# Optimization experiments

Hardware: AMD Instinct MI355X
Metric: run time of the kernel (lower is better)

The kernel has to match this reference:

```python
import jax, jax.numpy as jnp
import numpy as np

N = 50000
E_RAND = 800000
IN, HID, OUT = 128, 64, 40
HEADS = (2, 1, 1)
NEG_SLOPE = 0.2


def setup_inputs() -> dict:
    key = jax.random.key(0)
    ks = jax.random.split(key, 16)
    # random edges with src != dst, then append self-loops (remove+add_self_loop)
    src_r = jax.random.randint(ks[0], (E_RAND,), 0, N)
    off = jax.random.randint(ks[1], (E_RAND,), 1, N)
    dst_r = (src_r + off) % N
    loops = jnp.arange(N)
    src = jnp.concatenate([src_r, loops]).astype(jnp.int64)
    dst = jnp.concatenate([dst_r, loops]).astype(jnp.int64)
    in_feat = jax.random.normal(ks[2], (N, IN), dtype=jnp.float32)

    def lin(k, fan_in, fan_out):
        return jax.random.normal(k, (fan_in, fan_out), dtype=jnp.float32) / np.sqrt(fan_in)

    H0, H1, H2 = HEADS
    # layer 0: in=IN, out=HID, heads=H0
    W0 = lin(ks[3], IN, H0 * HID)
    al0 = jax.random.normal(ks[4], (H0, HID), dtype=jnp.float32) * 0.1
    ar0 = jax.random.normal(ks[5], (H0, HID), dtype=jnp.float32) * 0.1
    b0 = jnp.zeros((H0 * HID,), dtype=jnp.float32)
    # layer 1: in=HID*H0, out=HID, heads=H1
    W1 = lin(ks[6], HID * H0, H1 * HID)
    al1 = jax.random.normal(ks[7], (H1, HID), dtype=jnp.float32) * 0.1
    ar1 = jax.random.normal(ks[8], (H1, HID), dtype=jnp.float32) * 0.1
    b1 = jnp.zeros((H1 * HID,), dtype=jnp.float32)
    # layer 2: in=HID*H1, out=OUT, heads=H2
    W2 = lin(ks[9], HID * H1, H2 * OUT)
    al2 = jax.random.normal(ks[10], (H2, OUT), dtype=jnp.float32) * 0.1
    ar2 = jax.random.normal(ks[11], (H2, OUT), dtype=jnp.float32) * 0.1
    b2 = jnp.zeros((H2 * OUT,), dtype=jnp.float32)
    return {"in_feat": in_feat, "src": src, "dst": dst,
            "W0": W0, "al0": al0, "ar0": ar0, "b0": b0,
            "W1": W1, "al1": al1, "ar1": ar1, "b1": b1,
            "W2": W2, "al2": al2, "ar2": ar2, "b2": b2}


def _gat_layer(x, src, dst, W, al, ar, b):
    # x: [N, Fin]; W: [Fin, H*D]; al/ar: [H, D]; b: [H*D]
    H, D = al.shape
    feat = (x @ W).reshape(-1, H, D)                 # [N, H, D]
    el = jnp.sum(feat * al, axis=-1)                 # [N, H]
    er = jnp.sum(feat * ar, axis=-1)                 # [N, H]
    e = jax.nn.leaky_relu(el[src] + er[dst], NEG_SLOPE)  # [E, H]
    m = jax.ops.segment_max(e, dst, num_segments=x.shape[0])
    ee = jnp.exp(e - jax.lax.stop_gradient(m)[dst])
    s = jax.ops.segment_sum(ee, dst, num_segments=x.shape[0])
    alpha = ee / s[dst]                              # softmax over in-edges per dst
    out = jax.ops.segment_sum(feat[src] * alpha[:, :, None], dst,
                              num_segments=x.shape[0])  # [N, H, D]
    return out + b.reshape(1, H, D)


def reference(in_feat, src, dst, W0, al0, ar0, b0, W1, al1, ar1, b1, W2, al2, ar2, b2):
    h = _gat_layer(in_feat, src, dst, W0, al0, ar0, b0).reshape(in_feat.shape[0], -1)  # flatten(1)
    h = _gat_layer(h, src, dst, W1, al1, ar1, b1).mean(axis=1)                          # mean over heads
    h = _gat_layer(h, src, dst, W2, al2, ar2, b2).reshape(in_feat.shape[0], -1)         # flatten(1)
    return h
```

## Files before the change

kernel.cpp:

```cpp
#include <hip/hip_runtime.h>
#include <hip/hip_fp16.h>
#include <math.h>

#define NEG_SLOPE 0.2f

typedef _Float16 h8 __attribute__((ext_vector_type(8)));
typedef float f4 __attribute__((ext_vector_type(4)));


__device__ inline float2 up2(unsigned u) {
    __half2 h;
    __builtin_memcpy(&h, &u, 4);
    return __half22float2(h);
}
__device__ inline unsigned pk2(float a, float b) {
    __half2 h = __floats2half2_rn(a, b);
    unsigned u;
    __builtin_memcpy(&u, &h, 4);
    return u;
}
__device__ inline void fma8(float* acc, const uint4& v, float p) {
    float2 f;
    f = up2(v.x); acc[0] += f.x * p; acc[1] += f.y * p;
    f = up2(v.y); acc[2] += f.x * p; acc[3] += f.y * p;
    f = up2(v.z); acc[4] += f.x * p; acc[5] += f.y * p;
    f = up2(v.w); acc[6] += f.x * p; acc[7] += f.y * p;
}
__device__ inline float dot4(const float4& a, const float4& b) {
    return a.x * b.x + a.y * b.y + a.z * b.z + a.w * b.w;
}


__global__ __launch_bounds__(256) void degree_hist_rank(const int* __restrict__ dst,
                                                        int* __restrict__ deg,
                                                        int* __restrict__ rank, int E) {
    int e = blockIdx.x * blockDim.x + threadIdx.x;
    if (e >= E) return;
    int d = __builtin_nontemporal_load(&dst[e]);
    int r = atomicAdd(&deg[d], 1);
    __builtin_nontemporal_store(r, &rank[e]);
}

__global__ __launch_bounds__(256) void scan_block_sums(const int* __restrict__ in,
                                                       int* __restrict__ partial, int n) {
    int i = blockIdx.x * 256 + threadIdx.x;
    int v = (i < n) ? in[i] : 0;
#pragma unroll
    for (int off = 32; off; off >>= 1) v += __shfl_xor(v, off);
    __shared__ int wsum[4];
    if ((threadIdx.x & 63) == 0) wsum[threadIdx.x >> 6] = v;
    __syncthreads();
    if (threadIdx.x == 0) partial[blockIdx.x] = wsum[0] + wsum[1] + wsum[2] + wsum[3];
}

__global__ __launch_bounds__(256) void scan_offsets(const int* __restrict__ partial,
                                                    int* __restrict__ partial_scan,
                                                    int* __restrict__ total_out, int nb,
                                                    const float* __restrict__ al2,
                                                    const float* __restrict__ ar2,
                                                    float* __restrict__ al2p,
                                                    float* __restrict__ ar2p) {
    __shared__ int buf[256];
    int t = threadIdx.x;
    int v = (t < nb) ? partial[t] : 0;
    buf[t] = v;
    __syncthreads();
    for (int off = 1; off < 256; off <<= 1) {
        int x = (t >= off) ? buf[t - off] : 0;
        __syncthreads();
        buf[t] += x;
        __syncthreads();
    }
    partial_scan[t] = buf[t] - v;
    if (t == 255) *total_out = buf[255];
    if (t < 64) {
        al2p[t] = (t < 40) ? al2[t] : 0.f;
        ar2p[t] = (t < 40) ? ar2[t] : 0.f;
    }
}

__global__ __launch_bounds__(256) void scan_final(const int* __restrict__ in,
                                                  const int* __restrict__ partial_scan,
                                                  int* __restrict__ out, int n) {
    __shared__ int buf[256];
    int t = threadIdx.x;
    int i = blockIdx.x * 256 + t;
    int v = (i < n) ? in[i] : 0;
    buf[t] = v;
    __syncthreads();
    for (int off = 1; off < 256; off <<= 1) {
        int x = (t >= off) ? buf[t - off] : 0;
        __syncthreads();
        buf[t] += x;
        __syncthreads();
    }
    if (i < n) out[i] = partial_scan[blockIdx.x] + buf[t] - v;
}

__global__ __launch_bounds__(256) void scatter_rank(const int* __restrict__ src,
                                                    const int* __restrict__ dst,
                                                    const int* __restrict__ rank,
                                                    const int* __restrict__ row_start,
                                                    int* __restrict__ csr_src, int E) {
    int e = blockIdx.x * blockDim.x + threadIdx.x;
    if (e >= E) return;
    int d = __builtin_nontemporal_load(&dst[e]);
    int s = __builtin_nontemporal_load(&src[e]);
    int r = __builtin_nontemporal_load(&rank[e]);
    csr_src[row_start[d] + r] = s;
}


__global__ __launch_bounds__(256) void pack_w(const float* __restrict__ W0,
                                              const float* __restrict__ W1,
                                              const float* __restrict__ W2,
                                              __half* __restrict__ P0,
                                              __half* __restrict__ P1,
                                              __half* __restrict__ P2) {
    int b = blockIdx.x;
    const float* W;
    __half* P;
    int K, M, Msrc;
    if (b < 8) {
        W = W0; P = P0; K = 128; M = 128; Msrc = 128;
    } else if (b < 12) {
        W = W1; P = P1; K = 128; M = 64; Msrc = 64; b -= 8;
    } else {
        W = W2; P = P2; K = 64; M = 64; Msrc = 40; b -= 12;
    }
    int t = b * 256 + threadIdx.x;
    int nk8 = K >> 3;
    if (t >= M * nk8) return;
    int m = t % M, k8 = t / M;
    int k = k8 * 8;
    int c = m >> 4, s = k >> 5, hi = (k >> 3) & 3, lane = hi * 16 + (m & 15);
    float v[8];
#pragma unroll
    for (int i = 0; i < 8; ++i)
        v[i] = (m < Msrc) ? W[(size_t)(k + i) * Msrc + m] : 0.f;
    uint4 o;
    o.x = pk2(v[0], v[1]);
    o.y = pk2(v[2], v[3]);
    o.z = pk2(v[4], v[5]);
    o.w = pk2(v[6], v[7]);
    *(uint4*)(P + (size_t)((c * (K >> 5) + s) * 64 + lane) * 8) = o;
}


template <int K, int M, int H, bool A16>
__global__ __launch_bounds__(256) void gemm_mfma(const void* __restrict__ xin,
                                                 const __half* __restrict__ Wp,
                                                 const float* __restrict__ al,
                                                 const float* __restrict__ ar,
                                                 __half* __restrict__ outh,
                                                 float* __restrict__ el,
                                                 float* __restrict__ er, int N) {
    constexpr int KS = K / 32;
    constexpr int CF = M / 16;
    constexpr int LDT = 133;
    constexpr int CH8 = M / 8;
    constexpr int NC8 = CH8 / 4;
    __shared__ float tl[4 * 16 * LDT];
    const int tid = threadIdx.x;
    const int wid = tid >> 6, lane = tid & 63;
    const int lhi = lane >> 4, llo = lane & 15;
    const int rowbase = blockIdx.x * 64 + wid * 16;
    float* wt = tl + wid * 16 * LDT;

    f4 acc[CF];
#pragma unroll
    for (int c = 0; c < CF; ++c) acc[c] = f4{0.f, 0.f, 0.f, 0.f};

    const int arow = rowbase + llo;
    const bool aval = arow < N;
#pragma unroll
    for (int s = 0; s < KS; ++s) {
        h8 a = {};
        if (aval) {
            if constexpr (A16) {
                const __half* xp = (const __half*)xin + (size_t)arow * K + s * 32 + lhi * 8;
                a = *(const h8*)xp;
            } else {
                const float4* xp = (const float4*)((const float*)xin + (size_t)arow * K +
                                                   s * 32 + lhi * 8);
                float4 x0 = xp[0];
                float4 x1 = xp[1];
                a[0] = (_Float16)x0.x; a[1] = (_Float16)x0.y;
                a[2] = (_Float16)x0.z; a[3] = (_Float16)x0.w;
                a[4] = (_Float16)x1.x; a[5] = (_Float16)x1.y;
                a[6] = (_Float16)x1.z; a[7] = (_Float16)x1.w;
            }
        }
#pragma unroll
        for (int c = 0; c < CF; ++c) {
            h8 b = *(const h8*)(Wp + (size_t)((c * KS + s) * 64 + lane) * 8);
            acc[c] = __builtin_amdgcn_mfma_f32_16x16x32_f16(a, b, acc[c], 0, 0, 0);
        }
    }

#pragma unroll
    for (int c = 0; c < CF; ++c) {
#pragma unroll
        for (int r = 0; r < 4; ++r)
            wt[(lhi * 4 + r) * LDT + c * 16 + llo] = acc[c][r];
    }

    const int rrow = lane >> 2;
    const int q = lane & 3;
    const int grow = rowbase + rrow;
    float elp[H], erp[H];
#pragma unroll
    for (int h = 0; h < H; ++h) { elp[h] = 0.f; erp[h] = 0.f; }
    const float4* al4 = (const float4*)al;
    const float4* ar4 = (const float4*)ar;
#pragma unroll
    for (int i = 0; i < NC8; ++i) {
        int j8 = q + 4 * i;
        float4 v0 = *(float4*)&wt[rrow * LDT + 8 * j8];
        float4 v1 = *(float4*)&wt[rrow * LDT + 8 * j8 + 4];
        int h = (H == 2 && i >= NC8 / 2) ? 1 : 0;
        float4 a0 = al4[2 * j8], a1 = al4[2 * j8 + 1];
        float4 r0 = ar4[2 * j8], r1 = ar4[2 * j8 + 1];
        elp[h] += dot4(v0, a0) + dot4(v1, a1);
        erp[h] += dot4(v0, r0) + dot4(v1, r1);
        if (grow < N) {
            uint4 pkv;
            pkv.x = pk2(v0.x, v0.y);
            pkv.y = pk2(v0.z, v0.w);
            pkv.z = pk2(v1.x, v1.y);
            pkv.w = pk2(v1.z, v1.w);
            *(uint4*)(outh + (size_t)grow * M + 8 * j8) = pkv;
        }
    }
#pragma unroll
    for (int h = 0; h < H; ++h) {
#pragma unroll
        for (int off = 1; off < 4; off <<= 1) {
            elp[h] += __shfl_xor(elp[h], off);
            erp[h] += __shfl_xor(erp[h], off);
        }
    }
    if (q == 0 && grow < N) {
        if constexpr (H == 2) {
            *(float2*)&el[(size_t)grow * 2] = float2{elp[0], elp[1]};
            *(float2*)&er[(size_t)grow * 2] = float2{erp[0], erp[1]};
        } else {
            el[grow] = elp[0];
            er[grow] = erp[0];
        }
    }
}


template <int H, int D, int FSTRIDE, int T, bool OUT16>
__global__ __launch_bounds__(256) void gat_aggregate(const __half* __restrict__ feat,
                                                     const float* __restrict__ el,
                                                     const float* __restrict__ er,
                                                     const int* __restrict__ row_start,
                                                     const int* __restrict__ csr_src,
                                                     const float* __restrict__ bias,
                                                     void* __restrict__ out, int N) {
    constexpr int NLp = FSTRIDE / 8;
    constexpr int Gn = 64 / NLp;
    constexpr int BATCH = Gn * T;
    constexpr int WL = (H * D) / 8;
    static_assert(BATCH <= 64 && 64 % NLp == 0, "layout");
    int dstn = (blockIdx.x * blockDim.x + threadIdx.x) >> 6;
    int lane = threadIdx.x & 63;
    if (dstn >= N) return;
    int beg = row_start[dstn], end = row_start[dstn + 1];
    int cnt = end - beg;

    float er_d[H];
#pragma unroll
    for (int h = 0; h < H; ++h) er_d[h] = er[(size_t)dstn * H + h];

    float ssum[H];
    float acc8[8];
#pragma unroll
    for (int h = 0; h < H; ++h) ssum[h] = 0.f;
#pragma unroll
    for (int i = 0; i < 8; ++i) acc8[i] = 0.f;

    const int g = lane / NLp;
    const int ln = lane % NLp;

    auto gather = [&](int s_reg, const float p_reg[H], int j, int limit) {
        uint4 v[T];
#pragma unroll
        for (int t = 0; t < T; ++t) {
            if (j + Gn * t < limit) {
                int sj = __shfl(s_reg, j + Gn * t + g);
                v[t] = ((const uint4*)(feat + (size_t)sj * FSTRIDE))[ln];
            }
        }
#pragma unroll
        for (int t = 0; t < T; ++t) {
            if (j + Gn * t < limit) {
                int slot = j + Gn * t + g;
                float pj = __shfl(p_reg[0], slot);
                if constexpr (H == 2) {
                    float pj1 = __shfl(p_reg[1], slot);
                    pj = (ln >= 8) ? pj1 : pj;
                }
                fma8(acc8, v[t], pj);
            }
        }
    };

    if (cnt <= 64) {
        int idx = beg + lane;
        bool valid = idx < end;
        int s = valid ? csr_src[idx] : csr_src[beg];
        float ev[H], p[H];
        if constexpr (H == 2) {
            float2 e2 = ((const float2*)el)[s];
            ev[0] = e2.x + er_d[0];
            ev[1] = e2.y + er_d[1];
        } else {
            ev[0] = el[s] + er_d[0];
        }
#pragma unroll
        for (int h = 0; h < H; ++h) {
            float e = ev[h];
            e = (e > 0.f) ? e : NEG_SLOPE * e;
            p[h] = valid ? __expf(e) : 0.f;
            ssum[h] = p[h];
        }
        for (int j = 0; j < cnt; j += BATCH) gather(s, p, j, cnt);
    } else {
        for (int base = beg; base < end; base += 64) {
            int idx = base + lane;
            bool valid = idx < end;
            int s = valid ? csr_src[idx] : csr_src[beg];
            float p[H];
            float ev[H];
            if constexpr (H == 2) {
                float2 e2 = ((const float2*)el)[s];
                ev[0] = e2.x + er_d[0];
                ev[1] = e2.y + er_d[1];
            } else {
                ev[0] = el[s] + er_d[0];
            }
#pragma unroll
            for (int h = 0; h < H; ++h) {
                float e = ev[h];
                e = (e > 0.f) ? e : NEG_SLOPE * e;
                p[h] = valid ? __expf(e) : 0.f;
                ssum[h] += p[h];
            }
            int ccnt = (end - base < 64) ? end - base : 64;
            for (int j = 0; j < ccnt; j += BATCH) gather(s, p, j, ccnt);
        }
    }

#pragma unroll
    for (int h = 0; h < H; ++h)
#pragma unroll
        for (int off = 32; off; off >>= 1) ssum[h] += __shfl_xor(ssum[h], off);
#pragma unroll
    for (int i = 0; i < 8; ++i) {
#pragma unroll
        for (int off = NLp; off < 64; off <<= 1) acc8[i] += __shfl_xor(acc8[i], off);
    }
    if (lane < WL) {
        float inv;
        if constexpr (H == 2) inv = 1.f / ((lane >= 8) ? ssum[1] : ssum[0]);
        else inv = 1.f / ssum[0];
        const float4* bp = (const float4*)bias;
        float4 bv0 = bp[2 * lane], bv1 = bp[2 * lane + 1];
        float4 o0, o1;
        o0.x = acc8[0] * inv + bv0.x; o0.y = acc8[1] * inv + bv0.y;
        o0.z = acc8[2] * inv + bv0.z; o0.w = acc8[3] * inv + bv0.w;
        o1.x = acc8[4] * inv + bv1.x; o1.y = acc8[5] * inv + bv1.y;
        o1.z = acc8[6] * inv + bv1.z; o1.w = acc8[7] * inv + bv1.w;
        if constexpr (OUT16) {
            __half* op = (__half*)out + (size_t)dstn * (H * D);
            uint4 pkv;
            pkv.x = pk2(o0.x, o0.y);
            pkv.y = pk2(o0.z, o0.w);
            pkv.z = pk2(o1.x, o1.y);
            pkv.w = pk2(o1.z, o1.w);
            ((uint4*)op)[lane] = pkv;
        } else {
            float4* op = (float4*)((float*)out + (size_t)dstn * (H * D));
            op[2 * lane] = o0;
            op[2 * lane + 1] = o1;
        }
    }
}


extern "C" void kernel_launch(void* const* d_in, const int* in_sizes, int n_in,
                              void* d_out, int out_size, void* d_ws, size_t ws_size,
                              hipStream_t stream) {
    const float* in_feat = (const float*)d_in[0];
    const int*   src     = (const int*)d_in[1];
    const int*   dst     = (const int*)d_in[2];
    const float* W0 = (const float*)d_in[3];
    const float* al0 = (const float*)d_in[4];
    const float* ar0 = (const float*)d_in[5];
    const float* b0 = (const float*)d_in[6];
    const float* W1 = (const float*)d_in[7];
    const float* al1 = (const float*)d_in[8];
    const float* ar1 = (const float*)d_in[9];
    const float* b1 = (const float*)d_in[10];
    const float* W2 = (const float*)d_in[11];
    const float* al2 = (const float*)d_in[12];
    const float* ar2 = (const float*)d_in[13];
    const float* b2 = (const float*)d_in[14];
    float* out = (float*)d_out;

    const int N = in_sizes[0] / 128;
    const int E = in_sizes[1];

    char* ws = (char*)d_ws;
    auto alloc = [&](size_t bytes) -> void* {
        void* p = (void*)ws;
        ws += (bytes + 255) & ~(size_t)255;
        return p;
    };
    int* deg       = (int*)alloc((size_t)N * 4);
    int* row_start = (int*)alloc((size_t)(N + 1) * 4);
    int* csr_src   = (int*)alloc((size_t)E * 4);
    int* rank      = (int*)alloc((size_t)E * 4);
    int* partial      = (int*)alloc(256 * 4);
    int* partial_scan = (int*)alloc(256 * 4);
    __half* feat   = (__half*)alloc((size_t)N * 128 * 2);
    float* el      = (float*)alloc((size_t)N * 2 * 4);
    float* er      = (float*)alloc((size_t)N * 2 * 4);
    __half* h0h    = (__half*)alloc((size_t)N * 128 * 2);
    __half* h1h    = (__half*)alloc((size_t)N * 64 * 2);
    __half* Wp0    = (__half*)alloc((size_t)128 * 128 * 2);
    __half* Wp1    = (__half*)alloc((size_t)128 * 64 * 2);
    __half* Wp2    = (__half*)alloc((size_t)64 * 64 * 2);
    float* al2p    = (float*)alloc(64 * 4);
    float* ar2p    = (float*)alloc(64 * 4);

    hipMemsetAsync(deg, 0, (size_t)N * 4, stream);

    int egrid = (E + 255) / 256;
    int nb = (N + 255) / 256;

    pack_w<<<14, 256, 0, stream>>>(W0, W1, W2, Wp0, Wp1, Wp2);
    degree_hist_rank<<<egrid, 256, 0, stream>>>(dst, deg, rank, E);
    scan_block_sums<<<nb, 256, 0, stream>>>(deg, partial, N);
    scan_offsets<<<1, 256, 0, stream>>>(partial, partial_scan, &row_start[N], nb,
                                        al2, ar2, al2p, ar2p);
    scan_final<<<nb, 256, 0, stream>>>(deg, partial_scan, row_start, N);
    scatter_rank<<<egrid, 256, 0, stream>>>(src, dst, rank, row_start, csr_src, E);

    int ngrid = (N * 64 + 255) / 256;
    int mgrid = (N + 63) / 64;

    gemm_mfma<128, 128, 2, false><<<mgrid, 256, 0, stream>>>(in_feat, Wp0, al0, ar0, feat, el, er, N);
    gat_aggregate<2, 64, 128, 4, true><<<ngrid, 256, 0, stream>>>(feat, el, er, row_start, csr_src, b0, h0h, N);

    gemm_mfma<128, 64, 1, true><<<mgrid, 256, 0, stream>>>(h0h, Wp1, al1, ar1, feat, el, er, N);
    gat_aggregate<1, 64, 64, 4, true><<<ngrid, 256, 0, stream>>>(feat, el, er, row_start, csr_src, b1, h1h, N);

    gemm_mfma<64, 64, 1, true><<<mgrid, 256, 0, stream>>>(h1h, Wp2, al2p, ar2p, feat, el, er, N);
    gat_aggregate<1, 40, 64, 4, false><<<ngrid, 256, 0, stream>>>(feat, el, er, row_start, csr_src, b2, out, N);
}
```

Measured before the change: 283.0 us.

## Process two destination nodes per wavefront in GAT aggregation and fuse prep kernels

The aggregation kernel now assigns two destination nodes per 64-lane wavefront, with each half-wave handling one node's in-edges in 32-edge chunks, and the gather batch depth T rises from 4 to 8. With about 17 edges per node, this is meant to cut the idle lanes and per-node overhead of the one-node-per-wave layout. The weight packing, degree zeroing and attention-vector padding move into one prep kernel, replacing a memset and a separate launch. The single-block scan_offsets kernel is removed because each scan_final2 block sums its preceding block partials itself. In exchange, the two half-waves diverge when their nodes have different degrees, and the larger batch adds register pressure.

```diff
diff --git a/kernel.cpp b/kernel.cpp
--- a/kernel.cpp
+++ b/kernel.cpp
@@ -28,6 +28,59 @@
 }
 __device__ inline float dot4(const float4& a, const float4& b) {
     return a.x * b.x + a.y * b.y + a.z * b.z + a.w * b.w;
+}
+
+
+__global__ __launch_bounds__(256) void prep(const float* __restrict__ W0,
+                                            const float* __restrict__ W1,
+                                            const float* __restrict__ W2,
+                                            const float* __restrict__ al2,
+                                            const float* __restrict__ ar2,
+                                            __half* __restrict__ P0,
+                                            __half* __restrict__ P1,
+                                            __half* __restrict__ P2,
+                                            float* __restrict__ al2p,
+                                            float* __restrict__ ar2p,
+                                            int* __restrict__ deg, int N) {
+    int b = blockIdx.x;
+    int gtid = b * 256 + threadIdx.x;
+    for (int i = gtid; i < N; i += gridDim.x * 256) deg[i] = 0;
+
+    if (b < 14) {
+        const float* W;
+        __half* P;
+        int K, M, Msrc, lb = b;
+        if (lb < 8) {
+            W = W0; P = P0; K = 128; M = 128; Msrc = 128;
+        } else if (lb < 12) {
+            W = W1; P = P1; K = 128; M = 64; Msrc = 64; lb -= 8;
+        } else {
+            W = W2; P = P2; K = 64; M = 64; Msrc = 40; lb -= 12;
+        }
+        int t = lb * 256 + threadIdx.x;
+        int nk8 = K >> 3;
+        if (t < M * nk8) {
+            int m = t % M, k8 = t / M;
+            int k = k8 * 8;
+            int c = m >> 4, s = k >> 5, hi = (k >> 3) & 3, lane = hi * 16 + (m & 15);
+            float v[8];
+#pragma unroll
+            for (int i = 0; i < 8; ++i)
+                v[i] = (m < Msrc) ? W[(size_t)(k + i) * Msrc + m] : 0.f;
+            uint4 o;
+            o.x = pk2(v[0], v[1]);
+            o.y = pk2(v[2], v[3]);
+            o.z = pk2(v[4], v[5]);
+            o.w = pk2(v[6], v[7]);
+            *(uint4*)(P + (size_t)((c * (K >> 5) + s) * 64 + lane) * 8) = o;
+        }
+    } else if (b == 14) {
+        int t = threadIdx.x;
+        if (t < 64) {
+            al2p[t] = (t < 40) ? al2[t] : 0.f;
+            ar2p[t] = (t < 40) ? ar2[t] : 0.f;
+        }
+    }
 }
 
 
@@ -53,36 +106,11 @@
     if (threadIdx.x == 0) partial[blockIdx.x] = wsum[0] + wsum[1] + wsum[2] + wsum[3];
 }
 
-__global__ __launch_bounds__(256) void scan_offsets(const int* __restrict__ partial,
-                                                    int* __restrict__ partial_scan,
-                                                    int* __restrict__ total_out, int nb,
-                                                    const float* __restrict__ al2,
-                                                    const float* __restrict__ ar2,
-                                                    float* __restrict__ al2p,
-                                                    float* __restrict__ ar2p) {
+__global__ __launch_bounds__(256) void scan_final2(const int* __restrict__ in,
+                                                   const int* __restrict__ partial,
+                                                   int* __restrict__ out, int n) {
     __shared__ int buf[256];
-    int t = threadIdx.x;
-    int v = (t < nb) ? partial[t] : 0;
-    buf[t] = v;
-    __syncthreads();
-    for (int off = 1; off < 256; off <<= 1) {
-        int x = (t >= off) ? buf[t - off] : 0;
-        __syncthreads();
-        buf[t] += x;
-        __syncthreads();
-    }
-    partial_scan[t] = buf[t] - v;
-    if (t == 255) *total_out = buf[255];
-    if (t < 64) {
-        al2p[t] = (t < 40) ? al2[t] : 0.f;
-        ar2p[t] = (t < 40) ? ar2[t] : 0.f;
-    }
-}
-
-__global__ __launch_bounds__(256) void scan_final(const int* __restrict__ in,
-                                                  const int* __restrict__ partial_scan,
-                                                  int* __restrict__ out, int n) {
-    __shared__ int buf[256];
+    __shared__ int wsum[4];
     int t = threadIdx.x;
     int i = blockIdx.x * 256 + t;
     int v = (i < n) ? in[i] : 0;
@@ -94,7 +122,15 @@
         buf[t] += x;
         __syncthreads();
     }
-    if (i < n) out[i] = partial_scan[blockIdx.x] + buf[t] - v;
+    int incl = buf[t];
+    int pv = (t < blockIdx.x) ? partial[t] : 0;
+#pragma unroll
+    for (int off = 32; off; off >>= 1) pv += __shfl_xor(pv, off);
+    if ((t & 63) == 0) wsum[t >> 6] = pv;
+    __syncthreads();
+    int pre = wsum[0] + wsum[1] + wsum[2] + wsum[3];
+    if (i < n) out[i] = pre + incl - v;
+    if (i == n - 1) out[n] = pre + incl;
 }
 
 __global__ __launch_bounds__(256) void scatter_rank(const int* __restrict__ src,
@@ -108,42 +144,6 @@
     int s = __builtin_nontemporal_load(&src[e]);
     int r = __builtin_nontemporal_load(&rank[e]);
     csr_src[row_start[d] + r] = s;
-}
-
-
-__global__ __launch_bounds__(256) void pack_w(const float* __restrict__ W0,
-                                              const float* __restrict__ W1,
-                                              const float* __restrict__ W2,
-                                              __half* __restrict__ P0,
-                                              __half* __restrict__ P1,
-                                              __half* __restrict__ P2) {
-    int b = blockIdx.x;
-    const float* W;
-    __half* P;
-    int K, M, Msrc;
-    if (b < 8) {
-        W = W0; P = P0; K = 128; M = 128; Msrc = 128;
-    } else if (b < 12) {
-        W = W1; P = P1; K = 128; M = 64; Msrc = 64; b -= 8;
-    } else {
-        W = W2; P = P2; K = 64; M = 64; Msrc = 40; b -= 12;
-    }
-    int t = b * 256 + threadIdx.x;
-    int nk8 = K >> 3;
-    if (t >= M * nk8) return;
-    int m = t % M, k8 = t / M;
-    int k = k8 * 8;
-    int c = m >> 4, s = k >> 5, hi = (k >> 3) & 3, lane = hi * 16 + (m & 15);
-    float v[8];
-#pragma unroll
-    for (int i = 0; i < 8; ++i)
-        v[i] = (m < Msrc) ? W[(size_t)(k + i) * Msrc + m] : 0.f;
-    uint4 o;
-    o.x = pk2(v[0], v[1]);
-    o.y = pk2(v[2], v[3]);
-    o.z = pk2(v[4], v[5]);
-    o.w = pk2(v[6], v[7]);
-    *(uint4*)(P + (size_t)((c * (K >> 5) + s) * 64 + lane) * 8) = o;
 }
 
 
@@ -253,27 +253,32 @@
 
 
 template <int H, int D, int FSTRIDE, int T, bool OUT16>
-__global__ __launch_bounds__(256) void gat_aggregate(const __half* __restrict__ feat,
-                                                     const float* __restrict__ el,
-                                                     const float* __restrict__ er,
-                                                     const int* __restrict__ row_start,
-                                                     const int* __restrict__ csr_src,
-                                                     const float* __restrict__ bias,
-                                                     void* __restrict__ out, int N) {
+__global__ __launch_bounds__(256) void gat_aggregate2(const __half* __restrict__ feat,
+                                                      const float* __restrict__ el,
+                                                      const float* __restrict__ er,
+                                                      const int* __restrict__ row_start,
+                                                      const int* __restrict__ csr_src,
+                                                      const float* __restrict__ bias,
+                                                      void* __restrict__ out, int N) {
     constexpr int NLp = FSTRIDE / 8;
-    constexpr int Gn = 64 / NLp;
-    constexpr int BATCH = Gn * T;
+    constexpr int GnH = 32 / NLp;
+    constexpr int BATCH = GnH * T;
     constexpr int WL = (H * D) / 8;
-    static_assert(BATCH <= 64 && 64 % NLp == 0, "layout");
-    int dstn = (blockIdx.x * blockDim.x + threadIdx.x) >> 6;
+    static_assert(32 % NLp == 0 && BATCH <= 32, "layout");
+    int pair = (blockIdx.x * blockDim.x + threadIdx.x) >> 6;
     int lane = threadIdx.x & 63;
-    if (dstn >= N) return;
-    int beg = row_start[dstn], end = row_start[dstn + 1];
+    if (pair * 2 >= N) return;
+    const int l32 = lane & 31;
+    const int hb = lane & 32;
+    const int dstn = pair * 2 + (lane >> 5);
+    const bool dval = dstn < N;
+    int beg = dval ? row_start[dstn] : 0;
+    int end = dval ? row_start[dstn + 1] : 0;
     int cnt = end - beg;
 
     float er_d[H];
 #pragma unroll
-    for (int h = 0; h < H; ++h) er_d[h] = er[(size_t)dstn * H + h];
+    for (int h = 0; h < H; ++h) er_d[h] = dval ? er[(size_t)dstn * H + h] : 0.f;
 
     float ssum[H];
     float acc8[8];
@@ -282,93 +287,83 @@
 #pragma unroll
     for (int i = 0; i < 8; ++i) acc8[i] = 0.f;
 
-    const int g = lane / NLp;
-    const int ln = lane % NLp;
-
-    auto gather = [&](int s_reg, const float p_reg[H], int j, int limit) {
-        uint4 v[T];
-#pragma unroll
-        for (int t = 0; t < T; ++t) {
-            if (j + Gn * t < limit) {
-                int sj = __shfl(s_reg, j + Gn * t + g);
-                v[t] = ((const uint4*)(feat + (size_t)sj * FSTRIDE))[ln];
-            }
-        }
-#pragma unroll
-        for (int t = 0; t < T; ++t) {
-            if (j + Gn * t < limit) {
-                int slot = j + Gn * t + g;
-                float pj = __shfl(p_reg[0], slot);
-                if constexpr (H == 2) {
-                    float pj1 = __shfl(p_reg[1], slot);
-                    pj = (ln >= 8) ? pj1 : pj;
-                }
-                fma8(acc8, v[t], pj);
-            }
-        }
-    };
-
-    if (cnt <= 64) {
-        int idx = beg + lane;
+    const int g = l32 / NLp;
+    const int ln = l32 % NLp;
+
+    int trips = (cnt + 31) >> 5;
+    {
+        int to = __shfl_xor(trips, 32);
+        trips = (to > trips) ? to : trips;
+    }
+
+    for (int it = 0; it < trips; ++it) {
+        int base = beg + it * 32;
+        int idx = base + l32;
         bool valid = idx < end;
-        int s = valid ? csr_src[idx] : csr_src[beg];
-        float ev[H], p[H];
+        int s = csr_src[valid ? idx : beg];
+        float p[H];
         if constexpr (H == 2) {
             float2 e2 = ((const float2*)el)[s];
-            ev[0] = e2.x + er_d[0];
-            ev[1] = e2.y + er_d[1];
+            float e0 = e2.x + er_d[0];
+            float e1 = e2.y + er_d[1];
+            e0 = (e0 > 0.f) ? e0 : NEG_SLOPE * e0;
+            e1 = (e1 > 0.f) ? e1 : NEG_SLOPE * e1;
+            p[0] = valid ? __expf(e0) : 0.f;
+            p[1] = valid ? __expf(e1) : 0.f;
+            ssum[0] += p[0];
+            ssum[1] += p[1];
         } else {
-            ev[0] = el[s] + er_d[0];
-        }
-#pragma unroll
-        for (int h = 0; h < H; ++h) {
-            float e = ev[h];
+            float e = el[s] + er_d[0];
             e = (e > 0.f) ? e : NEG_SLOPE * e;
-            p[h] = valid ? __expf(e) : 0.f;
-            ssum[h] = p[h];
-        }
-        for (int j = 0; j < cnt; j += BATCH) gather(s, p, j, cnt);
-    } else {
-        for (int base = beg; base < end; base += 64) {
-            int idx = base + lane;
-            bool valid = idx < end;
-            int s = valid ? csr_src[idx] : csr_src[beg];
-            float p[H];
-            float ev[H];
-            if constexpr (H == 2) {
-                float2 e2 = ((const float2*)el)[s];
-                ev[0] = e2.x + er_d[0];
-                ev[1] = e2.y + er_d[1];
-            } else {
-                ev[0] = el[s] + er_d[0];
+            p[0] = valid ? __expf(e) : 0.f;
+            ssum[0] += p[0];
+        }
+        int cc = end - base;
+        cc = (cc < 0) ? 0 : ((cc > 32) ? 32 : cc);
+        int ccm = cc;
+        {
+            int o = __shfl_xor(ccm, 32);
+            ccm = (o > ccm) ? o : ccm;
+        }
+        for (int j = 0; j < ccm; j += BATCH) {
+            uint4 v[T];
+#pragma unroll
+            for (int t = 0; t < T; ++t) {
+                if (j + GnH * t < cc) {
+                    int sj = __shfl(s, hb + j + GnH * t + g);
+                    v[t] = ((const uint4*)(feat + (size_t)sj * FSTRIDE))[ln];
+                }
             }
 #pragma unroll
-            for (int h = 0; h < H; ++h) {
-                float e = ev[h];
-                e = (e > 0.f) ? e : NEG_SLOPE * e;
-                p[h] = valid ? __expf(e) : 0.f;
-                ssum[h] += p[h];
+            for (int t = 0; t < T; ++t) {
+                if (j + GnH * t < cc) {
+                    int slot = hb + j + GnH * t + g;
+                    float pj = __shfl(p[0], slot);
+                    if constexpr (H == 2) {
+                        float pj1 = __shfl(p[1], slot);
+                        pj = (ln >= 8) ? pj1 : pj;
+                    }
+                    fma8(acc8, v[t], pj);
+                }
             }
-            int ccnt = (end - base < 64) ? end - base : 64;
-            for (int j = 0; j < ccnt; j += BATCH) gather(s, p, j, ccnt);
         }
     }
 
 #pragma unroll
     for (int h = 0; h < H; ++h)
 #pragma unroll
-        for (int off = 32; off; off >>= 1) ssum[h] += __shfl_xor(ssum[h], off);
+        for (int off = 16; off; off >>= 1) ssum[h] += __shfl_xor(ssum[h], off);
 #pragma unroll
     for (int i = 0; i < 8; ++i) {
 #pragma unroll
-        for (int off = NLp; off < 64; off <<= 1) acc8[i] += __shfl_xor(acc8[i], off);
-    }
-    if (lane < WL) {
+        for (int off = NLp; off < 32; off <<= 1) acc8[i] += __shfl_xor(acc8[i], off);
+    }
+    if (l32 < WL && dval) {
         float inv;
-        if constexpr (H == 2) inv = 1.f / ((lane >= 8) ? ssum[1] : ssum[0]);
+        if constexpr (H == 2) inv = 1.f / ((l32 >= 8) ? ssum[1] : ssum[0]);
         else inv = 1.f / ssum[0];
         const float4* bp = (const float4*)bias;
-        float4 bv0 = bp[2 * lane], bv1 = bp[2 * lane + 1];
+        float4 bv0 = bp[2 * l32], bv1 = bp[2 * l32 + 1];
         float4 o0, o1;
         o0.x = acc8[0] * inv + bv0.x; o0.y = acc8[1] * inv + bv0.y;
         o0.z = acc8[2] * inv + bv0.z; o0.w = acc8[3] * inv + bv0.w;
@@ -381,11 +376,11 @@
             pkv.y = pk2(o0.z, o0.w);
             pkv.z = pk2(o1.x, o1.y);
             pkv.w = pk2(o1.z, o1.w);
-            ((uint4*)op)[lane] = pkv;
+            ((uint4*)op)[l32] = pkv;
         } else {
             float4* op = (float4*)((float*)out + (size_t)dstn * (H * D));
-            op[2 * lane] = o0;
-            op[2 * lane + 1] = o1;
+            op[2 * l32] = o0;
+            op[2 * l32 + 1] = o1;
         }
     }
 }
@@ -424,8 +419,7 @@
     int* row_start = (int*)alloc((size_t)(N + 1) * 4);
     int* csr_src   = (int*)alloc((size_t)E * 4);
     int* rank      = (int*)alloc((size_t)E * 4);
-    int* partial      = (int*)alloc(256 * 4);
-    int* partial_scan = (int*)alloc(256 * 4);
+    int* partial   = (int*)alloc(256 * 4);
     __half* feat   = (__half*)alloc((size_t)N * 128 * 2);
     float* el      = (float*)alloc((size_t)N * 2 * 4);
     float* er      = (float*)alloc((size_t)N * 2 * 4);
@@ -437,28 +431,25 @@
     float* al2p    = (float*)alloc(64 * 4);
     float* ar2p    = (float*)alloc(64 * 4);
 
-    hipMemsetAsync(deg, 0, (size_t)N * 4, stream);
-
     int egrid = (E + 255) / 256;
     int nb = (N + 255) / 256;
 
-    pack_w<<<14, 256, 0, stream>>>(W0, W1, W2, Wp0, Wp1, Wp2);
+    prep<<<256, 256, 0, stream>>>(W0, W1, W2, al2, ar2, Wp0, Wp1, Wp2, al2p, ar2p, deg, N);
     degree_hist_rank<<<egrid, 256, 0, stream>>>(dst, deg, rank, E);
     scan_block_sums<<<nb, 256, 0, stream>>>(deg, partial, N);
-    scan_offsets<<<1, 256, 0, stream>>>(partial, partial_scan, &row_start[N], nb,
-                                        al2, ar2, al2p, ar2p);
-    scan_final<<<nb, 256, 0, stream>>>(deg, partial_scan, row_start, N);
+    scan_final2<<<nb, 256, 0, stream>>>(deg, partial, row_start, N);
     scatter_rank<<<egrid, 256, 0, stream>>>(src, dst, rank, row_start, csr_src, E);
 
-    int ngrid = (N * 64 + 255) / 256;
+    int npairs = (N + 1) / 2;
+    int pgrid = (npairs * 64 + 255) / 256;
     int mgrid = (N + 63) / 64;
 
     gemm_mfma<128, 128, 2, false><<<mgrid, 256, 0, stream>>>(in_feat, Wp0, al0, ar0, feat, el, er, N);
-    gat_aggregate<2, 64, 128, 4, true><<<ngrid, 256, 0, stream>>>(feat, el, er, row_start, csr_src, b0, h0h, N);
+    gat_aggregate2<2, 64, 128, 8, true><<<pgrid, 256, 0, stream>>>(feat, el, er, row_start, csr_src, b0, h0h, N);
 
     gemm_mfma<128, 64, 1, true><<<mgrid, 256, 0, stream>>>(h0h, Wp1, al1, ar1, feat, el, er, N);
-    gat_aggregate<1, 64, 64, 4, true><<<ngrid, 256, 0, stream>>>(feat, el, er, row_start, csr_src, b1, h1h, N);
+    gat_aggregate2<1, 64, 64, 8, true><<<pgrid, 256, 0, stream>>>(feat, el, er, row_start, csr_src, b1, h1h, N);
 
     gemm_mfma<64, 64, 1, true><<<mgrid, 256, 0, stream>>>(h1h, Wp2, al2p, ar2p, feat, el, er, N);
-    gat_aggregate<1, 40, 64, 4, false><<<ngrid, 256, 0, stream>>>(feat, el, er, row_start, csr_src, b2, out, N);
-}
+    gat_aggregate2<1, 40, 64, 8, false><<<pgrid, 256, 0, stream>>>(feat, el, er, row_start, csr_src, b2, out, N);
+}
```

Measured after the change: 281.5 us. Within noise of the previous version (-0.5%).
